# Kernel optimization log

Hardware: AMD Instinct MI355X
Metric: run time of the kernel (lower is better)

The kernel has to match this reference:

```python
import jax, jax.numpy as jnp
import numpy as np

B, T, D, V = 32, 384, 768, 32000
PAD = 1
THRESH = 0.95

def setup_inputs() -> dict:
    key = jax.random.key(0)
    ks = jax.random.split(key, 8)
    s = 1.0 / np.sqrt(D)
    sentence = jax.random.randint(ks[0], (B, T), 0, V)
    emb = jax.random.normal(ks[1], (V, D), jnp.float32) * 0.02
    emb = emb.at[PAD].set(0.0)  # padding_idx row is zero
    w_ih = jax.random.uniform(ks[2], (3 * D, D), jnp.float32, -s, s)
    w_hh = jax.random.uniform(ks[3], (3 * D, D), jnp.float32, -s, s)
    b_ih = jax.random.uniform(ks[4], (3 * D,), jnp.float32, -s, s)
    b_hh = jax.random.uniform(ks[5], (3 * D,), jnp.float32, -s, s)
    w_act = jax.random.uniform(ks[6], (D,), jnp.float32, -s, s)
    b_act = jnp.zeros((1,), jnp.float32)
    return dict(sentence=sentence, emb=emb, w_ih=w_ih, w_hh=w_hh,
                b_ih=b_ih, b_hh=b_hh, w_act=w_act, b_act=b_act)


def _gru(x, w_ih, w_hh, b_ih, b_hh):
    # x: [B,T,D] -> states [B,T,D]; PyTorch GRU cell math.
    xp = jnp.einsum('btd,ed->bte', x, w_ih) + b_ih  # [B,T,3D]

    def step(h, xt):
        hp = h @ w_hh.T + b_hh
        xr, xz, xn = jnp.split(xt, 3, axis=-1)
        hr, hz, hn = jnp.split(hp, 3, axis=-1)
        r = jax.nn.sigmoid(xr + hr)
        z = jax.nn.sigmoid(xz + hz)
        n = jnp.tanh(xn + r * hn)
        h_new = (1.0 - z) * n + z * h
        return h_new, h_new

    h0 = jnp.zeros((x.shape[0], w_hh.shape[1]), x.dtype)
    _, hs = jax.lax.scan(step, h0, jnp.swapaxes(xp, 0, 1))
    return jnp.swapaxes(hs, 0, 1)


def _forward(sentence, emb, w_ih, w_hh, b_ih, b_hh, w_act, b_act):
    x = emb[sentence]                                   # [B,T,D]
    states = _gru(x, w_ih, w_hh, b_ih, b_hh)            # [B,T,D]
    probs = jax.nn.sigmoid(states @ w_act + b_act)      # [B,T]

    # ACT-style halting: accumulate probs, emit a segment when sum > threshold.
    def halt_step(hsum, p):
        acc = hsum + p
        halted = acc > THRESH
        return jnp.where(halted, 0.0, acc), halted

    _, halted_t = jax.lax.scan(halt_step, jnp.zeros((B,), probs.dtype), probs.T)
    halted = halted_t.T                                 # [B,T] bool, True at last step of each segment
    h_i = halted.astype(jnp.int32)
    seg_id = jnp.cumsum(h_i, axis=1) - h_i              # exclusive cumsum: segment index per step

    segsum = jax.vmap(lambda v, s: jax.ops.segment_sum(v, s, num_segments=T))
    sum_p = segsum(probs, seg_id)                       # [B,T] per-segment prob sum
    sum_p_at = jnp.take_along_axis(sum_p, seg_id, axis=1)
    # last step of a segment gets weight p_last - stopgrad(sum_seg - 1)
    weights = jnp.where(halted, probs - jax.lax.stop_gradient(sum_p_at - 1.0), probs)
    seg_embs = segsum(states * weights[..., None], seg_id)  # [B,T,D]

    n_segs = h_i.sum(axis=1)                            # [B] completed segments
    valid = jnp.arange(T)[None, :] < n_segs[:, None]    # [B,T]
    embs = jnp.where(valid[..., None], seg_embs, 0.0)   # zero-pad incomplete slots
    embs = embs.reshape(B * T, D)                       # concat padded per-batch lists
    return embs, probs[..., None]


def reference(sentence, emb, w_ih, w_hh, b_ih, b_hh, w_act, b_act):
    return _forward(sentence, emb, w_ih, w_hh, b_ih, b_hh, w_act, b_act)
```

## Files before the change

kernel.cpp:

```cpp
#include <hip/hip_runtime.h>
#include <math.h>

#define BATCH 32
#define SEQT 384
#define DIM 768
#define D3 2304
#define NROWS (BATCH*SEQT)
#define VTHRESH 0.95f

typedef float  f32x4 __attribute__((ext_vector_type(4)));

#define OFF_XP   ((size_t)0)
#define SZ_XP    ((size_t)NROWS * D3 * 4)
#define OFF_ST   (OFF_XP + SZ_XP)
#define SZ_ST    ((size_t)NROWS * DIM * 4)
#define OFF_PR   (OFF_ST + SZ_ST)
#define SZ_PR    ((size_t)NROWS * 4)
#define OFF_WT   (OFF_PR + SZ_PR)
#define OFF_SS   (OFF_WT + SZ_PR)
#define OFF_SE   (OFF_SS + SZ_PR)
#define OFF_NS   (OFF_SE + SZ_PR)
#define OFF_HB   (OFF_NS + 256)
#define NBG 4
#define BPG 8
#define CPB 12
#define HCH 3
#define BGBYTES ((size_t)(DIM * HCH * 16))
#define SZ_HB   ((size_t)2 * NBG * BGBYTES)

#define DOT4(a,b) ((a).x*(b).x + (a).y*(b).y + (a).z*(b).z + (a).w*(b).w)

__global__ __launch_bounds__(256, 2) void k_xp(
    const int* __restrict__ sent, const float* __restrict__ emb,
    const float* __restrict__ w_ih, const float* __restrict__ b_ih,
    float* __restrict__ xp)
{
    __shared__ float As[16][132];
    __shared__ float Bs[16][132];
    const int tid = threadIdx.x;
    const int mt = blockIdx.x, nt = blockIdx.y;
    const int tx = tid & 15, ty = tid >> 4;
    const int lm = tid >> 2;
    const int lk = (tid & 3) << 2;

    const long arow0 = (long)sent[mt*128 + lm] * DIM;
    const long arow1 = (long)sent[mt*128 + lm + 64] * DIM;
    const float* b0p = w_ih + (size_t)(nt*128 + lm) * DIM;
    const float* b1p = w_ih + (size_t)(nt*128 + lm + 64) * DIM;

    float acc[8][8];
    #pragma unroll
    for (int i = 0; i < 8; ++i)
        #pragma unroll
        for (int j = 0; j < 8; ++j) acc[i][j] = 0.f;

    for (int k0 = 0; k0 < DIM; k0 += 16) {
        float4 a0 = *(const float4*)(emb + arow0 + k0 + lk);
        float4 a1 = *(const float4*)(emb + arow1 + k0 + lk);
        float4 b0 = *(const float4*)(b0p + k0 + lk);
        float4 b1 = *(const float4*)(b1p + k0 + lk);
        __syncthreads();
        As[lk+0][lm] = a0.x; As[lk+1][lm] = a0.y; As[lk+2][lm] = a0.z; As[lk+3][lm] = a0.w;
        As[lk+0][lm+64] = a1.x; As[lk+1][lm+64] = a1.y; As[lk+2][lm+64] = a1.z; As[lk+3][lm+64] = a1.w;
        Bs[lk+0][lm] = b0.x; Bs[lk+1][lm] = b0.y; Bs[lk+2][lm] = b0.z; Bs[lk+3][lm] = b0.w;
        Bs[lk+0][lm+64] = b1.x; Bs[lk+1][lm+64] = b1.y; Bs[lk+2][lm+64] = b1.z; Bs[lk+3][lm+64] = b1.w;
        __syncthreads();
        #pragma unroll
        for (int k = 0; k < 16; ++k) {
            float4 av0 = *(const float4*)&As[k][ty*8];
            float4 av1 = *(const float4*)&As[k][ty*8+4];
            float4 bv0 = *(const float4*)&Bs[k][tx*8];
            float4 bv1 = *(const float4*)&Bs[k][tx*8+4];
            float a[8] = {av0.x,av0.y,av0.z,av0.w,av1.x,av1.y,av1.z,av1.w};
            float b[8] = {bv0.x,bv0.y,bv0.z,bv0.w,bv1.x,bv1.y,bv1.z,bv1.w};
            #pragma unroll
            for (int i = 0; i < 8; ++i)
                #pragma unroll
                for (int j = 0; j < 8; ++j)
                    acc[i][j] += a[i]*b[j];
        }
    }

    const int m0 = mt*128 + ty*8;
    const int n0 = nt*128 + tx*8;
    float4 bi0 = *(const float4*)(b_ih + n0);
    float4 bi1 = *(const float4*)(b_ih + n0 + 4);
    #pragma unroll
    for (int i = 0; i < 8; ++i) {
        float4 v0, v1;
        v0.x = acc[i][0] + bi0.x; v0.y = acc[i][1] + bi0.y;
        v0.z = acc[i][2] + bi0.z; v0.w = acc[i][3] + bi0.w;
        v1.x = acc[i][4] + bi1.x; v1.y = acc[i][5] + bi1.y;
        v1.z = acc[i][6] + bi1.z; v1.w = acc[i][7] + bi1.w;
        *(float4*)(xp + (size_t)(m0+i)*D3 + n0)     = v0;
        *(float4*)(xp + (size_t)(m0+i)*D3 + n0 + 4) = v1;
    }
}

#define HPITCH 772

__global__ __launch_bounds__(384, 1) void k_gru(
    const float* __restrict__ w_hh, const float* __restrict__ b_hh,
    const float* __restrict__ xp, float* __restrict__ states,
    char* __restrict__ hbuf)
{
    __shared__ float h_lds[2][BPG][HPITCH];

    const int tid = threadIdx.x;
    const int jb  = blockIdx.x & 63;
    const int bg  = blockIdx.x >> 6;
    const int j    = tid >> 6;
    const int lane = tid & 63;
    const int c    = lane & 31;
    const int bh   = lane >> 5;
    const int col  = jb*CPB + j*2 + bh;
    const int bloc = (c >> 2) & 7;
    const int batch = bg*BPG + bloc;

    float4 w4[3][6];
    #pragma unroll
    for (int g3 = 0; g3 < 3; ++g3) {
        const float* wr = w_hh + (size_t)(g3*DIM + col)*DIM + c*4;
        #pragma unroll
        for (int kk = 0; kk < 6; ++kk)
            w4[g3][kk] = *(const float4*)(wr + kk*128);
    }
    const float bhr = b_hh[col];
    const float bhz = b_hh[DIM + col];
    const float bhn = b_hh[2*DIM + col];

    int goff[6], ldsoff[6], lastm = 0;
    #pragma unroll
    for (int i = 0; i < 6; ++i) {
        int q = i*384 + tid;
        int cq = q/3, sq = q - 3*cq;
        goff[i]   = q << 4;
        ldsoff[i] = (3*sq)*HPITCH + cq;
        if (sq == 2) lastm |= (1<<i);
    }

    char* pb_par[2];
    pb_par[0] = hbuf + (size_t)(0*NBG + bg)*BGBYTES;
    pb_par[1] = hbuf + (size_t)(1*NBG + bg)*BGBYTES;

    const float* xq = xp + ((size_t)batch*SEQT)*D3 + col;

    float hold = 0.f;

    for (int t = 0; t < SEQT; ++t) {
        float xr = xq[0], xz = xq[DIM], xn = xq[2*DIM];
        xq += D3;

        if (t > 0) {
            const char* pb = pb_par[(t-1)&1];
            f32x4 ch[6];
            int need = 63;
            while (need) {
                #pragma unroll
                for (int k = 0; k < 6; ++k)
                    if (need & (1<<k)) {
                        const f32x4* ap = (const f32x4*)(pb + goff[k]);
                        asm volatile("global_load_dwordx4 %0, %1, off sc0 sc1"
                                     : "=v"(ch[k]) : "v"(ap));
                    }
                asm volatile("s_waitcnt vmcnt(0)" ::: "memory");
                __builtin_amdgcn_sched_barrier(0);
                #pragma unroll
                for (int k = 0; k < 6; ++k)
                    if ((need & (1<<k)) && __float_as_int(ch[k].w) == t)
                        need &= ~(1<<k);
                if (need) __builtin_amdgcn_s_sleep(1);
            }
            float* hb0 = &h_lds[t & 1][0][0];
            #pragma unroll
            for (int k = 0; k < 6; ++k) {
                hb0[ldsoff[k]]            = ch[k].x;
                hb0[ldsoff[k] + HPITCH]   = ch[k].y;
                if (!((lastm >> k) & 1))
                    hb0[ldsoff[k] + 2*HPITCH] = ch[k].z;
            }
        }
        __syncthreads();

        float ar = 0.f, az = 0.f, an = 0.f;
        if (t > 0) {
            float v[24];
            #pragma unroll
            for (int i = 0; i < 24; ++i) v[i] = 0.f;
            const float* hbase = &h_lds[t & 1][0][c*4];
            #pragma unroll
            for (int bb = 0; bb < 8; ++bb) {
                const float* hr = hbase + bb*HPITCH;
                #pragma unroll
                for (int kk = 0; kk < 6; ++kk) {
                    float4 h4 = *(const float4*)(hr + kk*128);
                    v[bb*3+0] += DOT4(h4, w4[0][kk]);
                    v[bb*3+1] += DOT4(h4, w4[1][kk]);
                    v[bb*3+2] += DOT4(h4, w4[2][kk]);
                }
            }
            #pragma unroll
            for (int i = 0; i < 12; ++i) {
                float send = (c & 16) ? v[i] : v[i+12];
                float keep = (c & 16) ? v[i+12] : v[i];
                v[i] = keep + __shfl_xor(send, 16);
            }
            #pragma unroll
            for (int i = 0; i < 6; ++i) {
                float send = (c & 8) ? v[i] : v[i+6];
                float keep = (c & 8) ? v[i+6] : v[i];
                v[i] = keep + __shfl_xor(send, 8);
            }
            #pragma unroll
            for (int i = 0; i < 3; ++i) {
                float send = (c & 4) ? v[i] : v[i+3];
                float keep = (c & 4) ? v[i+3] : v[i];
                v[i] = keep + __shfl_xor(send, 4);
            }
            #pragma unroll
            for (int i = 0; i < 3; ++i) v[i] += __shfl_xor(v[i], 2);
            #pragma unroll
            for (int i = 0; i < 3; ++i) v[i] += __shfl_xor(v[i], 1);
            ar = v[0]; az = v[1]; an = v[2];
        }

        float rg = 1.f / (1.f + expf(-(xr + ar + bhr)));
        float zg = 1.f / (1.f + expf(-(xz + az + bhz)));
        float ng = tanhf(xn + rg * (an + bhn));
        hold = (1.f - zg) * ng + zg * hold;

        {
            int s_pub = c >> 2;
            int bb0 = 3*s_pub;
            int basel = lane & 32;
            float p0 = __shfl(hold, basel + ((4*(bb0+0)) & 31));
            float p1 = __shfl(hold, basel + ((4*(bb0+1)) & 31));
            float p2 = __shfl(hold, basel + ((4*(bb0+2)) & 31));
            if (((c & 3) == 0) && (c < 12)) {
                f32x4 val;
                val.x = p0; val.y = p1; val.z = p2;
                val.w = __int_as_float(t + 1);
                f32x4* ap = (f32x4*)(pb_par[t & 1]
                                     + (size_t)(col*HCH + s_pub)*16);
                asm volatile("global_store_dwordx4 %0, %1, off sc0 sc1"
                             :: "v"(ap), "v"(val) : "memory");
            }
        }
        if ((c & 3) == 0)
            states[(size_t)(batch*SEQT + t)*DIM + col] = hold;
    }
}

__global__ __launch_bounds__(256, 4) void k_probs(
    const float* __restrict__ states, const float* __restrict__ w_act,
    const float* __restrict__ b_act, float* __restrict__ probs,
    float* __restrict__ out_probs)
{
    int row  = blockIdx.x*4 + (threadIdx.x >> 6);
    int lane = threadIdx.x & 63;
    const float* sr = states + (size_t)row * DIM;
    float s = 0.f;
    #pragma unroll
    for (int i = 0; i < 3; ++i) {
        float4 v = *(const float4*)(sr + i*256 + lane*4);
        float4 w = *(const float4*)(w_act + i*256 + lane*4);
        s += v.x*w.x + v.y*w.y + v.z*w.z + v.w*w.w;
    }
    #pragma unroll
    for (int off = 32; off > 0; off >>= 1) s += __shfl_xor(s, off);
    if (lane == 0) {
        float pv = 1.f / (1.f + expf(-(s + b_act[0])));
        probs[row]     = pv;
        out_probs[row] = pv;
    }
}

__global__ void k_scan(const float* __restrict__ probs, float* __restrict__ weights,
                       int* __restrict__ seg_start, int* __restrict__ seg_end,
                       int* __restrict__ n_segs)
{
    int b = threadIdx.x;
    if (b >= BATCH) return;
    float acc = 0.f;
    int s = 0, start = 0;
    for (int t0 = 0; t0 < SEQT; t0 += 4) {
        float4 p4 = *(const float4*)(probs + b*SEQT + t0);
        float pv[4] = {p4.x, p4.y, p4.z, p4.w};
        #pragma unroll
        for (int k = 0; k < 4; ++k) {
            int t = t0 + k;
            float pp = pv[k];
            acc += pp;
            float w = pp;
            if (acc > VTHRESH) {
                w = pp - (acc - 1.0f);
                seg_start[b*SEQT + s] = start;
                seg_end[b*SEQT + s]   = t;
                s++; start = t + 1; acc = 0.f;
            }
            weights[b*SEQT + t] = w;
        }
    }
    n_segs[b] = s;
}

__global__ __launch_bounds__(256, 4) void k_embs(
    const float* __restrict__ states, const float* __restrict__ weights,
    const int* __restrict__ seg_start, const int* __restrict__ seg_end,
    const int* __restrict__ n_segs, float* __restrict__ out)
{
    int r = blockIdx.x;
    int b = r / SEQT;
    int s = r - b*SEQT;
    int tid = threadIdx.x;
    float a0 = 0.f, a1 = 0.f, a2 = 0.f;
    if (s < n_segs[b]) {
        int st = seg_start[r], en = seg_end[r];
        for (int t = st; t <= en; ++t) {
            float w = weights[b*SEQT + t];
            const float* sp = states + (size_t)(b*SEQT + t) * DIM;
            a0 += w * sp[tid];
            a1 += w * sp[tid + 256];
            a2 += w * sp[tid + 512];
        }
    }
    float* o = out + (size_t)r * DIM;
    o[tid]       = a0;
    o[tid + 256] = a1;
    o[tid + 512] = a2;
}

__global__ void k_init(float* hb) {
    hb[blockIdx.x * 256 + threadIdx.x] = 0.f;
}

extern "C" void kernel_launch(void* const* d_in, const int* in_sizes, int n_in,
                              void* d_out, int out_size, void* d_ws, size_t ws_size,
                              hipStream_t stream)
{
    const int*   sent  = (const int*)d_in[0];
    const float* emb   = (const float*)d_in[1];
    const float* w_ih  = (const float*)d_in[2];
    const float* w_hh  = (const float*)d_in[3];
    const float* b_ih  = (const float*)d_in[4];
    const float* b_hh  = (const float*)d_in[5];
    const float* w_act = (const float*)d_in[6];
    const float* b_act = (const float*)d_in[7];
    float* out = (float*)d_out;

    char* ws = (char*)d_ws;
    float* xp      = (float*)(ws + OFF_XP);
    float* states  = (float*)(ws + OFF_ST);
    float* probs   = (float*)(ws + OFF_PR);
    float* weights = (float*)(ws + OFF_WT);
    int*   sstart  = (int*)(ws + OFF_SS);
    int*   send    = (int*)(ws + OFF_SE);
    int*   nsegs   = (int*)(ws + OFF_NS);
    char*  hbuf    = (char*)(ws + OFF_HB);

    k_init<<<288, 256, 0, stream>>>((float*)hbuf);
    k_xp<<<dim3(96, 18), 256, 0, stream>>>(sent, emb, w_ih, b_ih, xp);
    k_gru<<<256, 384, 0, stream>>>(w_hh, b_hh, xp, states, hbuf);
    k_probs<<<NROWS/4, 256, 0, stream>>>(states, w_act, b_act, probs,
                                         out + (size_t)NROWS * DIM);
    k_scan<<<1, 64, 0, stream>>>(probs, weights, sstart, send, nsegs);
    k_embs<<<NROWS, 256, 0, stream>>>(states, weights, sstart, send, nsegs, out);
}
```

Measured before the change: 2.728 ms.

## Interleave two batch groups per GRU block to overlap cross-block h exchange

```diff
diff --git a/kernel.cpp b/kernel.cpp
--- a/kernel.cpp
+++ b/kernel.cpp
@@ -23,7 +23,6 @@
 #define OFF_HB   (OFF_NS + 256)
 #define NBG 4
 #define BPG 8
-#define CPB 12
 #define HCH 3
 #define BGBYTES ((size_t)(DIM * HCH * 16))
 #define SZ_HB   ((size_t)2 * NBG * BGBYTES)
@@ -107,23 +106,23 @@
     __shared__ float h_lds[2][BPG][HPITCH];
 
     const int tid = threadIdx.x;
-    const int jb  = blockIdx.x & 63;
-    const int bg  = blockIdx.x >> 6;
+    const int jb  = blockIdx.x & 127;
+    const int pr  = blockIdx.x >> 7;
     const int j    = tid >> 6;
     const int lane = tid & 63;
-    const int c    = lane & 31;
-    const int bh   = lane >> 5;
-    const int col  = jb*CPB + j*2 + bh;
-    const int bloc = (c >> 2) & 7;
-    const int batch = bg*BPG + bloc;
-
-    float4 w4[3][6];
+    const int col  = jb*6 + j;
+    const int b8   = lane >> 3;
+    const int bgA  = pr*2, bgB = pr*2 + 1;
+    const int batchA = bgA*BPG + b8;
+    const int batchB = bgB*BPG + b8;
+
+    float4 w4[3][3];
     #pragma unroll
     for (int g3 = 0; g3 < 3; ++g3) {
-        const float* wr = w_hh + (size_t)(g3*DIM + col)*DIM + c*4;
+        const float* wr = w_hh + (size_t)(g3*DIM + col)*DIM + lane*12;
         #pragma unroll
-        for (int kk = 0; kk < 6; ++kk)
-            w4[g3][kk] = *(const float4*)(wr + kk*128);
+        for (int kk = 0; kk < 3; ++kk)
+            w4[g3][kk] = *(const float4*)(wr + kk*4);
     }
     const float bhr = b_hh[col];
     const float bhz = b_hh[DIM + col];
@@ -139,116 +138,175 @@
         if (sq == 2) lastm |= (1<<i);
     }
 
-    char* pb_par[2];
-    pb_par[0] = hbuf + (size_t)(0*NBG + bg)*BGBYTES;
-    pb_par[1] = hbuf + (size_t)(1*NBG + bg)*BGBYTES;
-
-    const float* xq = xp + ((size_t)batch*SEQT)*D3 + col;
-
-    float hold = 0.f;
-
-    for (int t = 0; t < SEQT; ++t) {
-        float xr = xq[0], xz = xq[DIM], xn = xq[2*DIM];
-        xq += D3;
-
-        if (t > 0) {
-            const char* pb = pb_par[(t-1)&1];
-            f32x4 ch[6];
-            int need = 63;
-            while (need) {
-                #pragma unroll
-                for (int k = 0; k < 6; ++k)
-                    if (need & (1<<k)) {
-                        const f32x4* ap = (const f32x4*)(pb + goff[k]);
-                        asm volatile("global_load_dwordx4 %0, %1, off sc0 sc1"
-                                     : "=v"(ch[k]) : "v"(ap));
-                    }
-                asm volatile("s_waitcnt vmcnt(0)" ::: "memory");
-                __builtin_amdgcn_sched_barrier(0);
-                #pragma unroll
-                for (int k = 0; k < 6; ++k)
-                    if ((need & (1<<k)) && __float_as_int(ch[k].w) == t)
-                        need &= ~(1<<k);
-                if (need) __builtin_amdgcn_s_sleep(1);
-            }
-            float* hb0 = &h_lds[t & 1][0][0];
-            #pragma unroll
-            for (int k = 0; k < 6; ++k) {
-                hb0[ldsoff[k]]            = ch[k].x;
-                hb0[ldsoff[k] + HPITCH]   = ch[k].y;
-                if (!((lastm >> k) & 1))
-                    hb0[ldsoff[k] + 2*HPITCH] = ch[k].z;
-            }
+    char* pbA[2]; char* pbB[2];
+    pbA[0] = hbuf + (size_t)(0*NBG + bgA)*BGBYTES;
+    pbA[1] = hbuf + (size_t)(1*NBG + bgA)*BGBYTES;
+    pbB[0] = hbuf + (size_t)(0*NBG + bgB)*BGBYTES;
+    pbB[1] = hbuf + (size_t)(1*NBG + bgB)*BGBYTES;
+
+    const float* xqA = xp + (size_t)batchA*SEQT*D3 + col;
+    const float* xqB = xp + (size_t)batchB*SEQT*D3 + col;
+
+    f32x4 chA[6], chB[6];
+
+#define ISSUE_POLLS(pb, ch)                                              \
+    {                                                                    \
+        _Pragma("unroll")                                                \
+        for (int k = 0; k < 6; ++k) {                                    \
+            const f32x4* ap = (const f32x4*)((pb) + goff[k]);            \
+            asm volatile("global_load_dwordx4 %0, %1, off sc0 sc1"       \
+                         : "=v"((ch)[k]) : "v"(ap));                     \
+        }                                                                \
+    }
+
+#define WAIT_FILL(pb, ch, hb0, tt)                                       \
+    {                                                                    \
+        asm volatile("s_waitcnt vmcnt(0)" ::: "memory");                 \
+        __builtin_amdgcn_sched_barrier(0);                               \
+        int need = 63;                                                   \
+        _Pragma("unroll")                                                \
+        for (int k = 0; k < 6; ++k)                                      \
+            if (__float_as_int((ch)[k].w) == (tt)) need &= ~(1<<k);      \
+        while (need) {                                                   \
+            _Pragma("unroll")                                            \
+            for (int k = 0; k < 6; ++k)                                  \
+                if (need & (1<<k)) {                                     \
+                    const f32x4* ap = (const f32x4*)((pb) + goff[k]);    \
+                    asm volatile("global_load_dwordx4 %0, %1, off sc0 sc1"\
+                                 : "=v"((ch)[k]) : "v"(ap));             \
+                }                                                        \
+            asm volatile("s_waitcnt vmcnt(0)" ::: "memory");             \
+            __builtin_amdgcn_sched_barrier(0);                           \
+            _Pragma("unroll")                                            \
+            for (int k = 0; k < 6; ++k)                                  \
+                if ((need & (1<<k)) && __float_as_int((ch)[k].w) == (tt))\
+                    need &= ~(1<<k);                                     \
+            if (need) __builtin_amdgcn_s_sleep(1);                       \
+        }                                                                \
+        _Pragma("unroll")                                                \
+        for (int k = 0; k < 6; ++k) {                                    \
+            (hb0)[ldsoff[k]]            = (ch)[k].x;                     \
+            (hb0)[ldsoff[k] + HPITCH]   = (ch)[k].y;                     \
+            if (!((lastm >> k) & 1))                                     \
+                (hb0)[ldsoff[k] + 2*HPITCH] = (ch)[k].z;                 \
+        }                                                                \
+    }
+
+#define GRU_STEP(hb, xr, xz, xn, hold)                                   \
+    {                                                                    \
+        float v[24];                                                     \
+        _Pragma("unroll")                                                \
+        for (int i = 0; i < 24; ++i) v[i] = 0.f;                         \
+        const float* hk = (hb) + lane*12;                                \
+        _Pragma("unroll")                                                \
+        for (int bb = 0; bb < 8; ++bb) {                                 \
+            const float* hr = hk + bb*HPITCH;                            \
+            float4 h0 = *(const float4*)(hr);                            \
+            float4 h1 = *(const float4*)(hr + 4);                        \
+            float4 h2 = *(const float4*)(hr + 8);                        \
+            v[bb*3+0] += DOT4(h0, w4[0][0]) + DOT4(h1, w4[0][1]) + DOT4(h2, w4[0][2]); \
+            v[bb*3+1] += DOT4(h0, w4[1][0]) + DOT4(h1, w4[1][1]) + DOT4(h2, w4[1][2]); \
+            v[bb*3+2] += DOT4(h0, w4[2][0]) + DOT4(h1, w4[2][1]) + DOT4(h2, w4[2][2]); \
+        }                                                                \
+        _Pragma("unroll")                                                \
+        for (int i = 0; i < 12; ++i) {                                   \
+            float send = (lane & 32) ? v[i] : v[i+12];                   \
+            float keep = (lane & 32) ? v[i+12] : v[i];                   \
+            v[i] = keep + __shfl_xor(send, 32);                          \
+        }                                                                \
+        _Pragma("unroll")                                                \
+        for (int i = 0; i < 6; ++i) {                                    \
+            float send = (lane & 16) ? v[i] : v[i+6];                    \
+            float keep = (lane & 16) ? v[i+6] : v[i];                    \
+            v[i] = keep + __shfl_xor(send, 16);                          \
+        }                                                                \
+        _Pragma("unroll")                                                \
+        for (int i = 0; i < 3; ++i) {                                    \
+            float send = (lane & 8) ? v[i] : v[i+3];                     \
+            float keep = (lane & 8) ? v[i+3] : v[i];                     \
+            v[i] = keep + __shfl_xor(send, 8);                           \
+        }                                                                \
+        _Pragma("unroll")                                                \
+        for (int i = 0; i < 3; ++i) v[i] += __shfl_xor(v[i], 4);         \
+        _Pragma("unroll")                                                \
+        for (int i = 0; i < 3; ++i) v[i] += __shfl_xor(v[i], 2);         \
+        _Pragma("unroll")                                                \
+        for (int i = 0; i < 3; ++i) v[i] += __shfl_xor(v[i], 1);         \
+        float rg = 1.f / (1.f + expf(-((xr) + v[0] + bhr)));             \
+        float zg = 1.f / (1.f + expf(-((xz) + v[1] + bhz)));             \
+        float ng = tanhf((xn) + rg * (v[2] + bhn));                      \
+        (hold) = (1.f - zg) * ng + zg * (hold);                          \
+    }
+
+#define PUBLISH(pb, hold, tt)                                            \
+    {                                                                    \
+        float p0 = __shfl((hold), (lane*24) & 63);                       \
+        float p1 = __shfl((hold), (lane*24 + 8) & 63);                   \
+        float p2 = __shfl((hold), (lane*24 + 16) & 63);                  \
+        if (lane < 3) {                                                  \
+            f32x4 val;                                                   \
+            val.x = p0; val.y = p1; val.z = p2;                          \
+            val.w = __int_as_float((tt) + 1);                            \
+            f32x4* ap = (f32x4*)((pb) + (size_t)(col*HCH + lane)*16);    \
+            asm volatile("global_store_dwordx4 %0, %1, off sc0 sc1"      \
+                         :: "v"(ap), "v"(val) : "memory");               \
+        }                                                                \
+    }
+
+    float holdA = 0.f, holdB = 0.f;
+
+    float xrA = xqA[0], xzA = xqA[DIM], xnA = xqA[2*DIM];
+    float xrB = xqB[0], xzB = xqB[DIM], xnB = xqB[2*DIM];
+    {
+        float rg = 1.f / (1.f + expf(-(xrA + bhr)));
+        float zg = 1.f / (1.f + expf(-(xzA + bhz)));
+        float ng = tanhf(xnA + rg * bhn);
+        holdA = (1.f - zg) * ng;
+    }
+    PUBLISH(pbA[0], holdA, 0);
+    if ((lane & 7) == 0)
+        states[(size_t)(batchA*SEQT + 0)*DIM + col] = holdA;
+    ISSUE_POLLS(pbA[0], chA);
+    {
+        float rg = 1.f / (1.f + expf(-(xrB + bhr)));
+        float zg = 1.f / (1.f + expf(-(xzB + bhz)));
+        float ng = tanhf(xnB + rg * bhn);
+        holdB = (1.f - zg) * ng;
+    }
+    PUBLISH(pbB[0], holdB, 0);
+    if ((lane & 7) == 0)
+        states[(size_t)(batchB*SEQT + 0)*DIM + col] = holdB;
+    xrA = xqA[(size_t)D3]; xzA = xqA[(size_t)D3 + DIM]; xnA = xqA[(size_t)D3 + 2*DIM];
+
+    for (int t = 1; t < SEQT; ++t) {
+        WAIT_FILL(pbA[(t-1)&1], chA, &h_lds[0][0][0], t);
+        __syncthreads();
+        ISSUE_POLLS(pbB[(t-1)&1], chB);
+        xrB = xqB[(size_t)t*D3];
+        xzB = xqB[(size_t)t*D3 + DIM];
+        xnB = xqB[(size_t)t*D3 + 2*DIM];
+        GRU_STEP(&h_lds[0][0][0], xrA, xzA, xnA, holdA);
+        PUBLISH(pbA[t&1], holdA, t);
+        if ((lane & 7) == 0)
+            states[(size_t)(batchA*SEQT + t)*DIM + col] = holdA;
+
+        WAIT_FILL(pbB[(t-1)&1], chB, &h_lds[1][0][0], t);
+        __syncthreads();
+        if (t + 1 < SEQT) {
+            ISSUE_POLLS(pbA[t&1], chA);
+            xrA = xqA[(size_t)(t+1)*D3];
+            xzA = xqA[(size_t)(t+1)*D3 + DIM];
+            xnA = xqA[(size_t)(t+1)*D3 + 2*DIM];
         }
-        __syncthreads();
-
-        float ar = 0.f, az = 0.f, an = 0.f;
-        if (t > 0) {
-            float v[24];
-            #pragma unroll
-            for (int i = 0; i < 24; ++i) v[i] = 0.f;
-            const float* hbase = &h_lds[t & 1][0][c*4];
-            #pragma unroll
-            for (int bb = 0; bb < 8; ++bb) {
-                const float* hr = hbase + bb*HPITCH;
-                #pragma unroll
-                for (int kk = 0; kk < 6; ++kk) {
-                    float4 h4 = *(const float4*)(hr + kk*128);
-                    v[bb*3+0] += DOT4(h4, w4[0][kk]);
-                    v[bb*3+1] += DOT4(h4, w4[1][kk]);
-                    v[bb*3+2] += DOT4(h4, w4[2][kk]);
-                }
-            }
-            #pragma unroll
-            for (int i = 0; i < 12; ++i) {
-                float send = (c & 16) ? v[i] : v[i+12];
-                float keep = (c & 16) ? v[i+12] : v[i];
-                v[i] = keep + __shfl_xor(send, 16);
-            }
-            #pragma unroll
-            for (int i = 0; i < 6; ++i) {
-                float send = (c & 8) ? v[i] : v[i+6];
-                float keep = (c & 8) ? v[i+6] : v[i];
-                v[i] = keep + __shfl_xor(send, 8);
-            }
-            #pragma unroll
-            for (int i = 0; i < 3; ++i) {
-                float send = (c & 4) ? v[i] : v[i+3];
-                float keep = (c & 4) ? v[i+3] : v[i];
-                v[i] = keep + __shfl_xor(send, 4);
-            }
-            #pragma unroll
-            for (int i = 0; i < 3; ++i) v[i] += __shfl_xor(v[i], 2);
-            #pragma unroll
-            for (int i = 0; i < 3; ++i) v[i] += __shfl_xor(v[i], 1);
-            ar = v[0]; az = v[1]; an = v[2];
-        }
-
-        float rg = 1.f / (1.f + expf(-(xr + ar + bhr)));
-        float zg = 1.f / (1.f + expf(-(xz + az + bhz)));
-        float ng = tanhf(xn + rg * (an + bhn));
-        hold = (1.f - zg) * ng + zg * hold;
-
-        {
-            int s_pub = c >> 2;
-            int bb0 = 3*s_pub;
-            int basel = lane & 32;
-            float p0 = __shfl(hold, basel + ((4*(bb0+0)) & 31));
-            float p1 = __shfl(hold, basel + ((4*(bb0+1)) & 31));
-            float p2 = __shfl(hold, basel + ((4*(bb0+2)) & 31));
-            if (((c & 3) == 0) && (c < 12)) {
-                f32x4 val;
-                val.x = p0; val.y = p1; val.z = p2;
-                val.w = __int_as_float(t + 1);
-                f32x4* ap = (f32x4*)(pb_par[t & 1]
-                                     + (size_t)(col*HCH + s_pub)*16);
-                asm volatile("global_store_dwordx4 %0, %1, off sc0 sc1"
-                             :: "v"(ap), "v"(val) : "memory");
-            }
-        }
-        if ((c & 3) == 0)
-            states[(size_t)(batch*SEQT + t)*DIM + col] = hold;
-    }
+        GRU_STEP(&h_lds[1][0][0], xrB, xzB, xnB, holdB);
+        PUBLISH(pbB[t&1], holdB, t);
+        if ((lane & 7) == 0)
+            states[(size_t)(batchB*SEQT + t)*DIM + col] = holdB;
+    }
+#undef ISSUE_POLLS
+#undef WAIT_FILL
+#undef GRU_STEP
+#undef PUBLISH
 }
 
 __global__ __launch_bounds__(256, 4) void k_probs(
```

After: 2.900 ms. 1.06x slower.

## Split GRU recurrence into 8 batch groups of 4 with prefetched polling

Applied to the files above, without the earlier changes.

```diff
diff --git a/kernel.cpp b/kernel.cpp
--- a/kernel.cpp
+++ b/kernel.cpp
@@ -21,10 +21,9 @@
 #define OFF_SE   (OFF_SS + SZ_PR)
 #define OFF_NS   (OFF_SE + SZ_PR)
 #define OFF_HB   (OFF_NS + 256)
-#define NBG 4
-#define BPG 8
-#define CPB 12
-#define HCH 3
+#define NBG 8
+#define BPG 4
+#define HCH 2
 #define BGBYTES ((size_t)(DIM * HCH * 16))
 #define SZ_HB   ((size_t)2 * NBG * BGBYTES)
 
@@ -99,7 +98,7 @@
 
 #define HPITCH 772
 
-__global__ __launch_bounds__(384, 1) void k_gru(
+__global__ __launch_bounds__(384, 3) void k_gru(
     const float* __restrict__ w_hh, const float* __restrict__ b_hh,
     const float* __restrict__ xp, float* __restrict__ states,
     char* __restrict__ hbuf)
@@ -113,8 +112,8 @@
     const int lane = tid & 63;
     const int c    = lane & 31;
     const int bh   = lane >> 5;
-    const int col  = jb*CPB + j*2 + bh;
-    const int bloc = (c >> 2) & 7;
+    const int col  = jb*12 + j*2 + bh;
+    const int bloc = ((c >> 4) & 1)*2 + ((c >> 3) & 1);
     const int batch = bg*BPG + bloc;
 
     float4 w4[3][6];
@@ -122,133 +121,168 @@
     for (int g3 = 0; g3 < 3; ++g3) {
         const float* wr = w_hh + (size_t)(g3*DIM + col)*DIM + c*4;
         #pragma unroll
-        for (int kk = 0; kk < 6; ++kk)
-            w4[g3][kk] = *(const float4*)(wr + kk*128);
+        for (int m = 0; m < 6; ++m)
+            w4[g3][m] = *(const float4*)(wr + m*128);
     }
     const float bhr = b_hh[col];
     const float bhz = b_hh[DIM + col];
     const float bhn = b_hh[2*DIM + col];
 
-    int goff[6], ldsoff[6], lastm = 0;
-    #pragma unroll
-    for (int i = 0; i < 6; ++i) {
+    int goff[4], ldsoff[4], onemask = 0;
+    #pragma unroll
+    for (int i = 0; i < 4; ++i) {
         int q = i*384 + tid;
-        int cq = q/3, sq = q - 3*cq;
+        int cq = q >> 1, sq = q & 1;
         goff[i]   = q << 4;
-        ldsoff[i] = (3*sq)*HPITCH + cq;
-        if (sq == 2) lastm |= (1<<i);
-    }
-
-    char* pb_par[2];
-    pb_par[0] = hbuf + (size_t)(0*NBG + bg)*BGBYTES;
-    pb_par[1] = hbuf + (size_t)(1*NBG + bg)*BGBYTES;
-
-    const float* xq = xp + ((size_t)batch*SEQT)*D3 + col;
+        ldsoff[i] = 3*sq*HPITCH + cq;
+        if (sq) onemask |= (1<<i);
+    }
+
+    char* pb[2];
+    pb[0] = hbuf + (size_t)(0*NBG + bg)*BGBYTES;
+    pb[1] = hbuf + (size_t)(1*NBG + bg)*BGBYTES;
+
+    const float* xq = xp + (size_t)batch*SEQT*D3 + col;
+
+    f32x4 ch[4];
+
+#define ISSUE_POLLS(pbx)                                                 \
+    {                                                                    \
+        _Pragma("unroll")                                                \
+        for (int k = 0; k < 4; ++k) {                                    \
+            const f32x4* ap = (const f32x4*)((pbx) + goff[k]);           \
+            asm volatile("global_load_dwordx4 %0, %1, off sc0 sc1"       \
+                         : "=v"(ch[k]) : "v"(ap));                       \
+        }                                                                \
+    }
+
+#define WAIT_FILL(pbx, hb0, tt)                                          \
+    {                                                                    \
+        asm volatile("s_waitcnt vmcnt(0)" ::: "memory");                 \
+        __builtin_amdgcn_sched_barrier(0);                               \
+        int need = 15;                                                   \
+        _Pragma("unroll")                                                \
+        for (int k = 0; k < 4; ++k)                                      \
+            if (__float_as_int(ch[k].w) == (tt)) need &= ~(1<<k);        \
+        while (need) {                                                   \
+            _Pragma("unroll")                                            \
+            for (int k = 0; k < 4; ++k)                                  \
+                if (need & (1<<k)) {                                     \
+                    const f32x4* ap = (const f32x4*)((pbx) + goff[k]);   \
+                    asm volatile("global_load_dwordx4 %0, %1, off sc0 sc1"\
+                                 : "=v"(ch[k]) : "v"(ap));               \
+                }                                                        \
+            asm volatile("s_waitcnt vmcnt(0)" ::: "memory");             \
+            __builtin_amdgcn_sched_barrier(0);                           \
+            _Pragma("unroll")                                            \
+            for (int k = 0; k < 4; ++k)                                  \
+                if ((need & (1<<k)) && __float_as_int(ch[k].w) == (tt))  \
+                    need &= ~(1<<k);                                     \
+            if (need) __builtin_amdgcn_s_sleep(1);                       \
+        }                                                                \
+        _Pragma("unroll")                                                \
+        for (int k = 0; k < 4; ++k) {                                    \
+            (hb0)[ldsoff[k]] = ch[k].x;                                  \
+            if (!((onemask >> k) & 1)) {                                 \
+                (hb0)[ldsoff[k] + HPITCH]   = ch[k].y;                   \
+                (hb0)[ldsoff[k] + 2*HPITCH] = ch[k].z;                   \
+            }                                                            \
+        }                                                                \
+    }
+
+#define GRU_GATES(xr, xz, xn, ar, az, an)                                \
+    {                                                                    \
+        float rg = 1.f / (1.f + expf(-((xr) + (ar) + bhr)));             \
+        float zg = 1.f / (1.f + expf(-((xz) + (az) + bhz)));             \
+        float ng = tanhf((xn) + rg * ((an) + bhn));                      \
+        hold = (1.f - zg) * ng + zg * hold;                              \
+    }
+
+#define PUBLISH(pbx, tt)                                                 \
+    {                                                                    \
+        int lb = lane & 32;                                              \
+        float pa = __shfl(hold, lb + 0);                                 \
+        float pbv = __shfl(hold, lb + 8);                                \
+        float pc = __shfl(hold, lb + 16);                                \
+        float pd = __shfl(hold, lb + 24);                                \
+        if (c < 2) {                                                     \
+            f32x4 val;                                                   \
+            if (c == 0) { val.x = pa; val.y = pbv; val.z = pc; }         \
+            else        { val.x = pd; val.y = 0.f; val.z = 0.f; }        \
+            val.w = __int_as_float((tt) + 1);                            \
+            f32x4* ap = (f32x4*)((pbx) + (size_t)(col*HCH + c)*16);      \
+            asm volatile("global_store_dwordx4 %0, %1, off sc0 sc1"      \
+                         :: "v"(ap), "v"(val) : "memory");               \
+        }                                                                \
+    }
 
     float hold = 0.f;
 
-    for (int t = 0; t < SEQT; ++t) {
+    {
         float xr = xq[0], xz = xq[DIM], xn = xq[2*DIM];
-        xq += D3;
-
-        if (t > 0) {
-            const char* pb = pb_par[(t-1)&1];
-            f32x4 ch[6];
-            int need = 63;
-            while (need) {
-                #pragma unroll
-                for (int k = 0; k < 6; ++k)
-                    if (need & (1<<k)) {
-                        const f32x4* ap = (const f32x4*)(pb + goff[k]);
-                        asm volatile("global_load_dwordx4 %0, %1, off sc0 sc1"
-                                     : "=v"(ch[k]) : "v"(ap));
-                    }
-                asm volatile("s_waitcnt vmcnt(0)" ::: "memory");
-                __builtin_amdgcn_sched_barrier(0);
-                #pragma unroll
-                for (int k = 0; k < 6; ++k)
-                    if ((need & (1<<k)) && __float_as_int(ch[k].w) == t)
-                        need &= ~(1<<k);
-                if (need) __builtin_amdgcn_s_sleep(1);
+        GRU_GATES(xr, xz, xn, 0.f, 0.f, 0.f);
+    }
+    PUBLISH(pb[0], 0);
+    if ((c & 7) == 0)
+        states[(size_t)(batch*SEQT + 0)*DIM + col] = hold;
+    ISSUE_POLLS(pb[0]);
+    float xr = xq[(size_t)D3], xz = xq[(size_t)D3 + DIM], xn = xq[(size_t)D3 + 2*DIM];
+
+    for (int t = 1; t < SEQT; ++t) {
+        float* hb0 = &h_lds[t & 1][0][0];
+        WAIT_FILL(pb[(t-1)&1], hb0, t);
+        __syncthreads();
+
+        float v[12];
+        #pragma unroll
+        for (int i = 0; i < 12; ++i) v[i] = 0.f;
+        const float* hk = hb0 + c*4;
+        #pragma unroll
+        for (int bb = 0; bb < 4; ++bb) {
+            const float* hr = hk + bb*HPITCH;
+            #pragma unroll
+            for (int m = 0; m < 6; ++m) {
+                float4 h4 = *(const float4*)(hr + m*128);
+                v[bb*3+0] += DOT4(h4, w4[0][m]);
+                v[bb*3+1] += DOT4(h4, w4[1][m]);
+                v[bb*3+2] += DOT4(h4, w4[2][m]);
             }
-            float* hb0 = &h_lds[t & 1][0][0];
-            #pragma unroll
-            for (int k = 0; k < 6; ++k) {
-                hb0[ldsoff[k]]            = ch[k].x;
-                hb0[ldsoff[k] + HPITCH]   = ch[k].y;
-                if (!((lastm >> k) & 1))
-                    hb0[ldsoff[k] + 2*HPITCH] = ch[k].z;
-            }
-        }
-        __syncthreads();
-
-        float ar = 0.f, az = 0.f, an = 0.f;
-        if (t > 0) {
-            float v[24];
-            #pragma unroll
-            for (int i = 0; i < 24; ++i) v[i] = 0.f;
-            const float* hbase = &h_lds[t & 1][0][c*4];
-            #pragma unroll
-            for (int bb = 0; bb < 8; ++bb) {
-                const float* hr = hbase + bb*HPITCH;
-                #pragma unroll
-                for (int kk = 0; kk < 6; ++kk) {
-                    float4 h4 = *(const float4*)(hr + kk*128);
-                    v[bb*3+0] += DOT4(h4, w4[0][kk]);
-                    v[bb*3+1] += DOT4(h4, w4[1][kk]);
-                    v[bb*3+2] += DOT4(h4, w4[2][kk]);
-                }
-            }
-            #pragma unroll
-            for (int i = 0; i < 12; ++i) {
-                float send = (c & 16) ? v[i] : v[i+12];
-                float keep = (c & 16) ? v[i+12] : v[i];
-                v[i] = keep + __shfl_xor(send, 16);
-            }
-            #pragma unroll
-            for (int i = 0; i < 6; ++i) {
-                float send = (c & 8) ? v[i] : v[i+6];
-                float keep = (c & 8) ? v[i+6] : v[i];
-                v[i] = keep + __shfl_xor(send, 8);
-            }
-            #pragma unroll
-            for (int i = 0; i < 3; ++i) {
-                float send = (c & 4) ? v[i] : v[i+3];
-                float keep = (c & 4) ? v[i+3] : v[i];
-                v[i] = keep + __shfl_xor(send, 4);
-            }
-            #pragma unroll
-            for (int i = 0; i < 3; ++i) v[i] += __shfl_xor(v[i], 2);
-            #pragma unroll
-            for (int i = 0; i < 3; ++i) v[i] += __shfl_xor(v[i], 1);
-            ar = v[0]; az = v[1]; an = v[2];
-        }
-
-        float rg = 1.f / (1.f + expf(-(xr + ar + bhr)));
-        float zg = 1.f / (1.f + expf(-(xz + az + bhz)));
-        float ng = tanhf(xn + rg * (an + bhn));
-        hold = (1.f - zg) * ng + zg * hold;
-
-        {
-            int s_pub = c >> 2;
-            int bb0 = 3*s_pub;
-            int basel = lane & 32;
-            float p0 = __shfl(hold, basel + ((4*(bb0+0)) & 31));
-            float p1 = __shfl(hold, basel + ((4*(bb0+1)) & 31));
-            float p2 = __shfl(hold, basel + ((4*(bb0+2)) & 31));
-            if (((c & 3) == 0) && (c < 12)) {
-                f32x4 val;
-                val.x = p0; val.y = p1; val.z = p2;
-                val.w = __int_as_float(t + 1);
-                f32x4* ap = (f32x4*)(pb_par[t & 1]
-                                     + (size_t)(col*HCH + s_pub)*16);
-                asm volatile("global_store_dwordx4 %0, %1, off sc0 sc1"
-                             :: "v"(ap), "v"(val) : "memory");
-            }
-        }
-        if ((c & 3) == 0)
+        }
+        #pragma unroll
+        for (int i = 0; i < 6; ++i) {
+            float send = (c & 16) ? v[i] : v[i+6];
+            float keep = (c & 16) ? v[i+6] : v[i];
+            v[i] = keep + __shfl_xor(send, 16);
+        }
+        #pragma unroll
+        for (int i = 0; i < 3; ++i) {
+            float send = (c & 8) ? v[i] : v[i+3];
+            float keep = (c & 8) ? v[i+3] : v[i];
+            v[i] = keep + __shfl_xor(send, 8);
+        }
+        #pragma unroll
+        for (int i = 0; i < 3; ++i) v[i] += __shfl_xor(v[i], 4);
+        #pragma unroll
+        for (int i = 0; i < 3; ++i) v[i] += __shfl_xor(v[i], 2);
+        #pragma unroll
+        for (int i = 0; i < 3; ++i) v[i] += __shfl_xor(v[i], 1);
+
+        GRU_GATES(xr, xz, xn, v[0], v[1], v[2]);
+        PUBLISH(pb[t&1], t);
+        if ((c & 7) == 0)
             states[(size_t)(batch*SEQT + t)*DIM + col] = hold;
-    }
+
+        if (t + 1 < SEQT) {
+            ISSUE_POLLS(pb[t&1]);
+            xr = xq[(size_t)(t+1)*D3];
+            xz = xq[(size_t)(t+1)*D3 + DIM];
+            xn = xq[(size_t)(t+1)*D3 + 2*DIM];
+        }
+    }
+#undef ISSUE_POLLS
+#undef WAIT_FILL
+#undef GRU_GATES
+#undef PUBLISH
 }
 
 __global__ __launch_bounds__(256, 4) void k_probs(
@@ -358,9 +392,9 @@
     int*   nsegs   = (int*)(ws + OFF_NS);
     char*  hbuf    = (char*)(ws + OFF_HB);
 
-    k_init<<<288, 256, 0, stream>>>((float*)hbuf);
+    k_init<<<384, 256, 0, stream>>>((float*)hbuf);
     k_xp<<<dim3(96, 18), 256, 0, stream>>>(sent, emb, w_ih, b_ih, xp);
-    k_gru<<<256, 384, 0, stream>>>(w_hh, b_hh, xp, states, hbuf);
+    k_gru<<<512, 384, 0, stream>>>(w_hh, b_hh, xp, states, hbuf);
     k_probs<<<NROWS/4, 256, 0, stream>>>(states, w_act, b_act, probs,
                                          out + (size_t)NROWS * DIM);
     k_scan<<<1, 64, 0, stream>>>(probs, weights, sstart, send, nsegs);
```

Result: slower. 3.704 ms (+35.8%).
